# Optimization experiments

Measured on AMD Instinct MI355X. Metric: run time of the kernel, lower is better.

The kernel has to match this reference:

```python
import jax, jax.numpy as jnp
import numpy as np

V, D, NL, K, B, L, FF = 32000, 512, 4, 32, 2, 1024, 2048


def _ln(x, g, b, eps=1e-5):
    m = jnp.mean(x, axis=-1, keepdims=True)
    v = jnp.mean((x - m) ** 2, axis=-1, keepdims=True)
    return (x - m) * jax.lax.rsqrt(v + eps) * g + b


def setup_inputs() -> dict:
    key = jax.random.key(0)
    ks = jax.random.split(key, 16)
    s = 0.02
    n = lambda k, shape: jax.random.normal(k, shape, jnp.float32) * s
    inp = {
        "tokens": jax.random.randint(ks[0], (B, L), 0, V),
        "embed": n(ks[1], (V, D)),
        "ln1_g": jnp.ones((NL, D)), "ln1_b": jnp.zeros((NL, D)),
        "cp_w1": n(ks[2], (NL, D, D)), "cp_b1": jnp.zeros((NL, D)),
        "cp_w2": n(ks[3], (NL, D, K)), "cp_b2": jnp.zeros((NL, K)),
        "pos_scale": 0.5 * jnp.ones((NL,)), "content_scale": 0.5 * jnp.ones((NL,)),
        "val_w": n(ks[4], (NL, D, D)), "val_b": jnp.zeros((NL, D)),
        "oln_g": jnp.ones((NL, D)), "oln_b": jnp.zeros((NL, D)),
        "out_w": n(ks[5], (NL, D, D)), "out_b": jnp.zeros((NL, D)),
        "ln2_g": jnp.ones((NL, D)), "ln2_b": jnp.zeros((NL, D)),
        "ffn_w1": n(ks[6], (NL, D, FF)), "ffn_b1": jnp.zeros((NL, FF)),
        "ffn_w2": n(ks[7], (NL, FF, D)), "ffn_b2": jnp.zeros((NL, D)),
        "no_g": jnp.ones((D,)), "no_b": jnp.zeros((D,)),
        "head_b": jnp.zeros((V,)),
    }
    return inp


def _forward(tokens, embed, ln1_g, ln1_b, cp_w1, cp_b1, cp_w2, cp_b2,
             pos_scale, content_scale, val_w, val_b, oln_g, oln_b, out_w, out_b,
             ln2_g, ln2_b, ffn_w1, ffn_b1, ffn_w2, ffn_b2, no_g, no_b, head_b):
    Bn, Ln = tokens.shape
    Kn = cp_b2.shape[1]
    # fixed positional phases (register_buffer in torch)
    freqs = 1.0 / 10000.0 ** (jnp.arange(Kn, dtype=jnp.float32) / Kn)
    pos_phase = jnp.arange(Ln, dtype=jnp.float32)[:, None] * freqs[None, :]  # [L,K]
    inv_norm = 1.0 / jnp.sqrt(jnp.arange(1, Ln + 1, dtype=jnp.float32) * Kn)[None, :, None]
    h = embed[tokens]  # [B,L,D]
    for i in range(ln1_g.shape[0]):
        # --- DualAddressingPhasor on normed input ---
        x = _ln(h, ln1_g[i], ln1_b[i])
        cp = jnp.tanh(jnp.tanh(x @ cp_w1[i] + cp_b1[i]) @ cp_w2[i] + cp_b2[i]) * jnp.pi  # [B,L,K]
        tp = pos_scale[i] * pos_phase[None] + content_scale[i] * cp
        v = x @ val_w[i] + val_b[i]  # [B,L,D]
        c, s_ = jnp.cos(tp), jnp.sin(tp)  # [B,L,K]
        mem_r = jnp.cumsum(c[..., None] * v[:, :, None, :], axis=1)  # [B,L,K,D]
        mem_i = jnp.cumsum(s_[..., None] * v[:, :, None, :], axis=1)
        retrieved = (jnp.einsum('blkd,blk->bld', mem_r, c)
                     + jnp.einsum('blkd,blk->bld', mem_i, s_)) * inv_norm
        # phasor returns x + to_out(retrieved); block adds it back to h
        h = h + x + (_ln(retrieved, oln_g[i], oln_b[i]) @ out_w[i] + out_b[i])
        # --- FFN ---
        y = _ln(h, ln2_g[i], ln2_b[i])
        h = h + jax.nn.gelu(y @ ffn_w1[i] + ffn_b1[i], approximate=False) @ ffn_w2[i] + ffn_b2[i]
    # tied output head: head.weight = embed.weight
    return _ln(h, no_g, no_b) @ embed.T + head_b


def reference(tokens, embed, ln1_g, ln1_b, cp_w1, cp_b1, cp_w2, cp_b2,
              pos_scale, content_scale, val_w, val_b, oln_g, oln_b, out_w, out_b,
              ln2_g, ln2_b, ffn_w1, ffn_b1, ffn_w2, ffn_b2, no_g, no_b, head_b):
    return _forward(tokens, embed, ln1_g, ln1_b, cp_w1, cp_b1, cp_w2, cp_b2,
                    pos_scale, content_scale, val_w, val_b, oln_g, oln_b, out_w, out_b,
                    ln2_g, ln2_b, ffn_w1, ffn_b1, ffn_w2, ffn_b2, no_g, no_b, head_b)
```

## Files before the change

kernel.cpp:

```cpp
#include <hip/hip_runtime.h>
#include <hip/hip_bf16.h>
#include <math.h>

#define V_  32000
#define D_  512
#define NL_ 4
#define K_  32
#define B_  2
#define L_  1024
#define FF_ 2048
#define MR_ (B_ * L_)

typedef __bf16 bf16_t;
typedef __bf16 bf16x8 __attribute__((ext_vector_type(8)));
typedef float  f32x4  __attribute__((ext_vector_type(4)));

#define FLAG_TANH   1
#define FLAG_GELU   2
#define FLAG_INV    8
#define FLAG_CAUSAL 16
#define FLAG_TANHLO 32

#define GLDS(gsrc, ldst) \
  __builtin_amdgcn_global_load_lds( \
      (const __attribute__((address_space(1))) unsigned int*)(const void*)(gsrc), \
      (__attribute__((address_space(3))) unsigned int*)(void*)(ldst), 16, 0, 0)

__global__ void gather_kernel(const int* __restrict__ tokens,
                              const float* __restrict__ embed,
                              float* __restrict__ h) {
    int row = blockIdx.x;
    int t = tokens[row];
    const float4* src = (const float4*)(embed + (size_t)t * D_);
    float4* dst = (float4*)(h + (size_t)row * D_);
    dst[threadIdx.x] = src[threadIdx.x];
}

__global__ __launch_bounds__(256) void cvt_kernel(const float* __restrict__ in,
                                                  bf16_t* __restrict__ out) {
    size_t i = ((size_t)blockIdx.x * 256 + threadIdx.x) * 8;
    float4 f0 = ((const float4*)(in + i))[0];
    float4 f1 = ((const float4*)(in + i))[1];
    bf16x8 ov;
    ov[0] = (bf16_t)f0.x; ov[1] = (bf16_t)f0.y;
    ov[2] = (bf16_t)f0.z; ov[3] = (bf16_t)f0.w;
    ov[4] = (bf16_t)f1.x; ov[5] = (bf16_t)f1.y;
    ov[6] = (bf16_t)f1.z; ov[7] = (bf16_t)f1.w;
    *(bf16x8*)(out + i) = ov;
}

__global__ void bconcat_kernel(const float* __restrict__ a,
                               const float* __restrict__ b,
                               float* __restrict__ o) {
    int i = blockIdx.x, t = threadIdx.x;
    o[(size_t)i * 2 * D_ + t]       = a[(size_t)i * D_ + t];
    o[(size_t)i * 2 * D_ + D_ + t]  = b[(size_t)i * D_ + t];
}

__global__ __launch_bounds__(256) void ln_kernel(const float* __restrict__ in,
                                                 const float* __restrict__ g,
                                                 const float* __restrict__ b,
                                                 float* __restrict__ outf,
                                                 bf16_t* __restrict__ outb) {
    int row = blockIdx.x, tid = threadIdx.x;
    const float* rp = in + (size_t)row * D_;
    float v0 = rp[tid], v1 = rp[tid + 256];
    float s = v0 + v1, q = v0 * v0 + v1 * v1;
#pragma unroll
    for (int o = 32; o > 0; o >>= 1) {
        s += __shfl_down(s, o, 64);
        q += __shfl_down(q, o, 64);
    }
    __shared__ float ss[4], sq[4];
    if ((tid & 63) == 0) { ss[tid >> 6] = s; sq[tid >> 6] = q; }
    __syncthreads();
    float ts = ss[0] + ss[1] + ss[2] + ss[3];
    float tq = sq[0] + sq[1] + sq[2] + sq[3];
    float mean = ts * (1.0f / D_);
    float var = tq * (1.0f / D_) - mean * mean;
    float rstd = rsqrtf(var + 1e-5f);
    float o0 = (v0 - mean) * rstd * g[tid] + b[tid];
    float o1 = (v1 - mean) * rstd * g[tid + 256] + b[tid + 256];
    if (outf) {
        outf[(size_t)row * D_ + tid]       = o0;
        outf[(size_t)row * D_ + tid + 256] = o1;
    }
    if (outb) {
        outb[(size_t)row * D_ + tid]       = (bf16_t)o0;
        outb[(size_t)row * D_ + tid + 256] = (bf16_t)o1;
    }
}

__global__ __launch_bounds__(256) void tconv_kernel(const float* __restrict__ in,
                                                    bf16_t* __restrict__ out,
                                                    int R, int C,
                                                    size_t inz, size_t outz) {
    __shared__ float t[32][33];
    const float* ip = in + (size_t)blockIdx.z * inz;
    bf16_t* op = out + (size_t)blockIdx.z * outz;
    int r0 = blockIdx.y * 32, c0 = blockIdx.x * 32;
    int tx = threadIdx.x & 31, ty = threadIdx.x >> 5;
#pragma unroll
    for (int rr = 0; rr < 4; ++rr)
        t[ty + rr * 8][tx] = ip[(size_t)(r0 + ty + rr * 8) * C + c0 + tx];
    __syncthreads();
#pragma unroll
    for (int rr = 0; rr < 4; ++rr)
        op[(size_t)(c0 + ty + rr * 8) * R + r0 + tx] = (bf16_t)t[tx][ty + rr * 8];
}

template<int BM, int BN, int NBUF, bool BF32>
__global__ __launch_bounds__(256) void mgemm(
    const bf16_t* __restrict__ A, const void* __restrict__ Bp,
    const float* __restrict__ bias, const float* __restrict__ res1,
    const float* __restrict__ res2, float* __restrict__ Cf,
    bf16_t* __restrict__ Cb, int M, int N, int Kd, int flags,
    long long strA, long long strB, long long strC, int swz) {
    __shared__ bf16_t sA[NBUF][BM * 32];
    __shared__ bf16_t sB[NBUF][BN * 32];
    const int tid = threadIdx.x;
    const int wave = tid >> 6, lane = tid & 63;
    const int lrow = lane & 15, quad = lane >> 4;
    int bx = blockIdx.x, by = blockIdx.y;
    if (swz) {
        int gx = gridDim.x, gy = gridDim.y;
        int nwg = gx * gy;
        int lid = by * gx + bx;
        int q = nwg >> 3, r = nwg & 7;
        int xcd = lid & 7, slot = lid >> 3;
        int base = (xcd < r) ? xcd * (q + 1) : r * (q + 1) + (xcd - r) * q;
        int nid = base + slot;
        bx = nid / gy;
        by = nid - bx * gy;
    }
    const int m0 = by * BM, n0 = bx * BN;
    const int z = blockIdx.z;
    A += (size_t)z * strA;
    const bf16_t* Bb = (const bf16_t*)Bp + (BF32 ? 0 : (size_t)z * strB);
    const float*  Bf = (const float*)Bp  + (BF32 ? (size_t)z * strB : 0);
    constexpr int TM = BM / 32, TN = BN / 32;
    const int wm = (wave >> 1) * (BM / 2), wn = (wave & 1) * (BN / 2);
    f32x4 acc[TM][TN] = {};

    if constexpr (BF32) {
        for (int k0 = 0; k0 < Kd; k0 += 32) {
#pragma unroll
            for (int rb = 0; rb < BM / 64; ++rb) {
                int rowblk = wave * (BM / 64) + rb;
                int ml = rowblk * 16 + (lane >> 2);
                int qs = (lane & 3) ^ ((ml >> 1) & 3);
                GLDS(A + (size_t)(m0 + ml) * Kd + k0 + qs * 8, &sA[0][rowblk * 512]);
            }
#pragma unroll
            for (int rb = 0; rb < (BN * 4) / 256; ++rb) {
                int s = rb * 256 + tid;
                int nl = s >> 2, ql = s & 3;
                int qs = ql ^ ((nl >> 1) & 3);
                const float* src = Bf + (size_t)(n0 + nl) * Kd + k0 + qs * 8;
                float4 f0 = ((const float4*)src)[0];
                float4 f1 = ((const float4*)src)[1];
                bf16x8 ov;
                ov[0] = (bf16_t)f0.x; ov[1] = (bf16_t)f0.y;
                ov[2] = (bf16_t)f0.z; ov[3] = (bf16_t)f0.w;
                ov[4] = (bf16_t)f1.x; ov[5] = (bf16_t)f1.y;
                ov[6] = (bf16_t)f1.z; ov[7] = (bf16_t)f1.w;
                *(bf16x8*)(&sB[0][s * 8]) = ov;
            }
            __syncthreads();
            bf16x8 af[TM], bv[TN];
#pragma unroll
            for (int i = 0; i < TM; ++i) {
                int row = wm + i * 16 + lrow;
                af[i] = *(const bf16x8*)(&sA[0][(row * 4 + (quad ^ ((row >> 1) & 3))) * 8]);
            }
#pragma unroll
            for (int j = 0; j < TN; ++j) {
                int rown = wn + j * 16 + lrow;
                bv[j] = *(const bf16x8*)(&sB[0][(rown * 4 + (quad ^ ((rown >> 1) & 3))) * 8]);
            }
#pragma unroll
            for (int i = 0; i < TM; ++i)
#pragma unroll
                for (int j = 0; j < TN; ++j)
                    acc[i][j] = __builtin_amdgcn_mfma_f32_16x16x32_bf16(af[i], bv[j], acc[i][j], 0, 0, 0);
            __syncthreads();
        }
    } else {
        int kend = Kd;
        if (flags & FLAG_CAUSAL) { int ke = m0 + BM; kend = ke < Kd ? ke : Kd; }
        const int nk = kend >> 5;
        constexpr int NLD = BM / 64 + BN / 64;
        auto stage = [&](int t) {
            const int buf = t & (NBUF - 1);
            const int k0 = t << 5;
#pragma unroll
            for (int rb = 0; rb < BM / 64; ++rb) {
                int rowblk = wave * (BM / 64) + rb;
                int ml = rowblk * 16 + (lane >> 2);
                int qs = (lane & 3) ^ ((ml >> 1) & 3);
                GLDS(A + (size_t)(m0 + ml) * Kd + k0 + qs * 8, &sA[buf][rowblk * 512]);
            }
#pragma unroll
            for (int rb = 0; rb < BN / 64; ++rb) {
                int rowblk = wave * (BN / 64) + rb;
                int nl = rowblk * 16 + (lane >> 2);
                int qs = (lane & 3) ^ ((nl >> 1) & 3);
                GLDS(Bb + (size_t)(n0 + nl) * Kd + k0 + qs * 8, &sB[buf][rowblk * 512]);
            }
        };
        for (int t = 0; t < NBUF - 1 && t < nk; ++t) stage(t);
        for (int t = 0; t < nk; ++t) {
            const int nxt = t + NBUF - 1;
            if (nxt < nk) stage(nxt);
            const int issued_last = (nxt < nk) ? nxt : nk - 1;
            const int ahead = issued_last - t;
            switch (ahead) {
              case 0: asm volatile("s_waitcnt vmcnt(0)" ::: "memory"); break;
              case 1: asm volatile("s_waitcnt vmcnt(%0)" :: "n"(1 * NLD) : "memory"); break;
              case 2: asm volatile("s_waitcnt vmcnt(%0)" :: "n"(2 * NLD) : "memory"); break;
              default: asm volatile("s_waitcnt vmcnt(%0)" :: "n"(3 * NLD) : "memory"); break;
            }
            __builtin_amdgcn_s_barrier();
            const int buf = t & (NBUF - 1);
            const bf16_t* sAc = sA[buf];
            const bf16_t* sBc = sB[buf];
            bf16x8 af[TM], bv[TN];
#pragma unroll
            for (int i = 0; i < TM; ++i) {
                int row = wm + i * 16 + lrow;
                af[i] = *(const bf16x8*)(sAc + (row * 4 + (quad ^ ((row >> 1) & 3))) * 8);
            }
#pragma unroll
            for (int j = 0; j < TN; ++j) {
                int rown = wn + j * 16 + lrow;
                bv[j] = *(const bf16x8*)(sBc + (rown * 4 + (quad ^ ((rown >> 1) & 3))) * 8);
            }
#pragma unroll
            for (int i = 0; i < TM; ++i)
#pragma unroll
                for (int j = 0; j < TN; ++j)
                    acc[i][j] = __builtin_amdgcn_mfma_f32_16x16x32_bf16(af[i], bv[j], acc[i][j], 0, 0, 0);
            asm volatile("s_waitcnt lgkmcnt(0)" ::: "memory");
            __builtin_amdgcn_s_barrier();
        }
    }

    const size_t zo = (size_t)z * strC;
#pragma unroll
    for (int i = 0; i < TM; ++i) {
#pragma unroll
        for (int reg = 0; reg < 4; ++reg) {
            int m = m0 + wm + i * 16 + quad * 4 + reg;
            float rs = (flags & FLAG_INV) ? rsqrtf((float)(m + 1) * (float)K_) : 1.0f;
#pragma unroll
            for (int j = 0; j < TN; ++j) {
                int n = n0 + wn + j * 16 + lrow;
                float vv = acc[i][j][reg];
                if (bias) vv += bias[n];
                vv *= rs;
                if (flags & FLAG_TANH) vv = tanhf(vv);
                else if (flags & FLAG_GELU) vv = 0.5f * vv * (1.0f + erff(vv * 0.7071067811865476f));
                else if (flags & FLAG_TANHLO) { if (n < D_) vv = tanhf(vv); }
                size_t idx = zo + (size_t)m * N + n;
                if (res1) vv += res1[idx];
                if (res2) vv += res2[idx];
                if (Cf) Cf[idx] = vv;
                if (Cb) Cb[idx] = (bf16_t)vv;
            }
        }
    }
}

__global__ void phase_kernel(const float* __restrict__ t1,
                             const float* __restrict__ w2,
                             const float* __restrict__ b2,
                             const float* __restrict__ ps,
                             const float* __restrict__ cs,
                             int layer,
                             float* __restrict__ cbuf,
                             float* __restrict__ sbuf) {
    int row = blockIdx.x;
    int l = row & (L_ - 1);
    int tid = threadIdx.x;
    int k = tid & 31, hh = tid >> 5;
    const float* tr = t1 + (size_t)row * (2 * D_);
    float acc = 0.f;
    for (int d = hh * 256; d < hh * 256 + 256; ++d)
        acc = fmaf(tr[d], w2[d * K_ + k], acc);
    __shared__ float red[64];
    red[tid] = acc;
    __syncthreads();
    if (hh == 0) {
        float zz = red[k] + red[k + 32] + b2[k];
        float cp = tanhf(zz) * 3.14159265358979323846f;
        float freq = expf(-(float)k * (9.210340371976184f / (float)K_));
        float tp = ps[layer] * (float)l * freq + cs[layer] * cp;
        cbuf[(size_t)row * K_ + k] = cosf(tp);
        sbuf[(size_t)row * K_ + k] = sinf(tp);
    }
}

__global__ __launch_bounds__(256) void score_kernel(const float* __restrict__ cbuf,
                                                    const float* __restrict__ sbuf,
                                                    bf16_t* __restrict__ Ab) {
    int b = blockIdx.z;
    int l0 = blockIdx.y * 16, j0 = blockIdx.x * 16;
    if (j0 > l0) return;
    int tx = threadIdx.x, ty = threadIdx.y;
    int tid = ty * 16 + tx;
    __shared__ float Cl[16][33], Sl[16][33], Cj[16][33], Sj[16][33];
    const float* cb = cbuf + (size_t)b * L_ * K_;
    const float* sb = sbuf + (size_t)b * L_ * K_;
    for (int q = tid; q < 16 * 32; q += 256) {
        int rr = q >> 5, kk = q & 31;
        Cl[rr][kk] = cb[(size_t)(l0 + rr) * K_ + kk];
        Sl[rr][kk] = sb[(size_t)(l0 + rr) * K_ + kk];
        Cj[rr][kk] = cb[(size_t)(j0 + rr) * K_ + kk];
        Sj[rr][kk] = sb[(size_t)(j0 + rr) * K_ + kk];
    }
    __syncthreads();
    int l = l0 + ty, j = j0 + tx;
    float acc = 0.f;
#pragma unroll
    for (int kk = 0; kk < 32; ++kk)
        acc += Cl[ty][kk] * Cj[tx][kk] + Sl[ty][kk] * Sj[tx][kk];
    Ab[((size_t)b * L_ + l) * L_ + j] = (bf16_t)((j <= l) ? acc : 0.f);
}

extern "C" void kernel_launch(void* const* d_in, const int* in_sizes, int n_in,
                              void* d_out, int out_size, void* d_ws, size_t ws_size,
                              hipStream_t stream) {
    const int*   tokens        = (const int*)d_in[0];
    const float* embed         = (const float*)d_in[1];
    const float* ln1_g         = (const float*)d_in[2];
    const float* ln1_b         = (const float*)d_in[3];
    const float* cp_w1         = (const float*)d_in[4];
    const float* cp_b1         = (const float*)d_in[5];
    const float* cp_w2         = (const float*)d_in[6];
    const float* cp_b2         = (const float*)d_in[7];
    const float* pos_scale     = (const float*)d_in[8];
    const float* content_scale = (const float*)d_in[9];
    const float* val_w         = (const float*)d_in[10];
    const float* val_b         = (const float*)d_in[11];
    const float* oln_g         = (const float*)d_in[12];
    const float* oln_b         = (const float*)d_in[13];
    const float* out_w         = (const float*)d_in[14];
    const float* out_b         = (const float*)d_in[15];
    const float* ln2_g         = (const float*)d_in[16];
    const float* ln2_b         = (const float*)d_in[17];
    const float* ffn_w1        = (const float*)d_in[18];
    const float* ffn_b1        = (const float*)d_in[19];
    const float* ffn_w2        = (const float*)d_in[20];
    const float* ffn_b2        = (const float*)d_in[21];
    const float* no_g          = (const float*)d_in[22];
    const float* no_b          = (const float*)d_in[23];
    const float* head_b        = (const float*)d_in[24];
    float* out = (float*)d_out;

    float* h   = out;
    float* x   = h  + (size_t)MR_ * D_;
    float* t1v = x  + (size_t)MR_ * D_;
    float* r   = t1v + (size_t)MR_ * 2 * D_;
    float* cb  = r  + (size_t)MR_ * D_;
    float* sb  = cb + (size_t)MR_ * K_;
    bf16_t* x_bf  = (bf16_t*)(sb + (size_t)MR_ * K_);
    bf16_t* r_bf  = x_bf  + (size_t)MR_ * D_;
    bf16_t* y_bf  = r_bf  + (size_t)MR_ * D_;
    bf16_t* ff_bf = y_bf  + (size_t)MR_ * D_;
    bf16_t* sc_bf = ff_bf + (size_t)MR_ * FF_;
    bf16_t* vT_bf = sc_bf + (size_t)B_ * L_ * L_;
    bf16_t* wvT   = vT_bf + (size_t)B_ * D_ * L_;
    bf16_t* owT   = wvT   + (size_t)NL_ * 2 * D_ * D_;
    bf16_t* f1T   = owT   + (size_t)NL_ * D_ * D_;
    bf16_t* f2T   = f1T   + (size_t)NL_ * FF_ * D_;
    float*  b1v   = (float*)((((uintptr_t)(f2T + (size_t)NL_ * D_ * FF_)) + 15) & ~(uintptr_t)15);
    bf16_t* hn_bf = (bf16_t*)d_ws;
    bf16_t* emb_bf = hn_bf + (size_t)MR_ * D_;
    const bool big_ws =
        ws_size >= ((size_t)MR_ * D_ + (size_t)V_ * D_) * sizeof(bf16_t);

    gather_kernel<<<MR_, 128, 0, stream>>>(tokens, embed, h);

    tconv_kernel<<<dim3(16, 16, NL_), 256, 0, stream>>>(cp_w1, wvT, D_, D_, (size_t)D_ * D_, (size_t)2 * D_ * D_);
    tconv_kernel<<<dim3(16, 16, NL_), 256, 0, stream>>>(val_w, wvT + (size_t)D_ * D_, D_, D_, (size_t)D_ * D_, (size_t)2 * D_ * D_);
    bconcat_kernel<<<NL_, 512, 0, stream>>>(cp_b1, val_b, b1v);
    tconv_kernel<<<dim3(16, 16, NL_), 256, 0, stream>>>(out_w, owT, D_, D_, (size_t)D_ * D_, (size_t)D_ * D_);
    tconv_kernel<<<dim3(64, 16, NL_), 256, 0, stream>>>(ffn_w1, f1T, D_, FF_, (size_t)D_ * FF_, (size_t)D_ * FF_);
    tconv_kernel<<<dim3(16, 64, NL_), 256, 0, stream>>>(ffn_w2, f2T, FF_, D_, (size_t)FF_ * D_, (size_t)FF_ * D_);
    if (big_ws)
        cvt_kernel<<<(V_ * D_) / 2048, 256, 0, stream>>>(embed, emb_bf);

    for (int i = 0; i < NL_; ++i) {
        ln_kernel<<<MR_, 256, 0, stream>>>(h, ln1_g + i * D_, ln1_b + i * D_, x, x_bf);
        mgemm<64, 64, 4, false><<<dim3(16, 32, 1), 256, 0, stream>>>(
            x_bf, wvT + (size_t)i * 2 * D_ * D_, b1v + (size_t)i * 2 * D_,
            nullptr, nullptr, t1v, nullptr, MR_, 2 * D_, D_, FLAG_TANHLO, 0, 0, 0, 1);
        phase_kernel<<<MR_, 64, 0, stream>>>(
            t1v, cp_w2 + (size_t)i * D_ * K_, cp_b2 + i * K_,
            pos_scale, content_scale, i, cb, sb);
        tconv_kernel<<<dim3(16, 32, B_), 256, 0, stream>>>(
            t1v + D_, vT_bf, L_, 2 * D_, (size_t)L_ * 2 * D_, (size_t)D_ * L_);
        score_kernel<<<dim3(L_ / 16, L_ / 16, B_), dim3(16, 16), 0, stream>>>(cb, sb, sc_bf);
        mgemm<64, 64, 4, false><<<dim3(8, 16, B_), 256, 0, stream>>>(
            sc_bf, vT_bf, nullptr, nullptr, nullptr, r, nullptr,
            L_, D_, L_, FLAG_INV | FLAG_CAUSAL,
            (long long)L_ * L_, (long long)D_ * L_, (long long)L_ * D_, 1);
        ln_kernel<<<MR_, 256, 0, stream>>>(r, oln_g + i * D_, oln_b + i * D_, nullptr, r_bf);
        mgemm<64, 64, 4, false><<<dim3(8, 32, 1), 256, 0, stream>>>(
            r_bf, owT + (size_t)i * D_ * D_, out_b + i * D_,
            h, x, h, nullptr, MR_, D_, D_, 0, 0, 0, 0, 1);
        ln_kernel<<<MR_, 256, 0, stream>>>(h, ln2_g + i * D_, ln2_b + i * D_, nullptr, y_bf);
        mgemm<128, 128, 4, false><<<dim3(16, 16, 1), 256, 0, stream>>>(
            y_bf, f1T + (size_t)i * FF_ * D_, ffn_b1 + i * FF_,
            nullptr, nullptr, nullptr, ff_bf, MR_, FF_, D_, FLAG_GELU, 0, 0, 0, 1);
        mgemm<64, 64, 4, false><<<dim3(8, 32, 1), 256, 0, stream>>>(
            ff_bf, f2T + (size_t)i * D_ * FF_, ffn_b2 + i * D_,
            h, nullptr, h, nullptr, MR_, D_, FF_, 0, 0, 0, 0, 1);
    }

    ln_kernel<<<MR_, 256, 0, stream>>>(h, no_g, no_b, nullptr, hn_bf);
    if (big_ws) {
        mgemm<128, 128, 2, false><<<dim3(V_ / 128, MR_ / 128, 1), 256, 0, stream>>>(
            hn_bf, emb_bf, head_b, nullptr, nullptr, out, nullptr,
            MR_, V_, D_, 0, 0, 0, 0, 1);
    } else {
        mgemm<128, 128, 1, true><<<dim3(V_ / 128, MR_ / 128, 1), 256, 0, stream>>>(
            hn_bf, embed, head_b, nullptr, nullptr, out, nullptr,
            MR_, V_, D_, 0, 0, 0, 0, 1);
    }
}
```

Before: 1.508 ms.

## Compute phasor score matrix with MFMA GEMM over packed bf16 cos/sin

The phase kernel now writes cos and sin as one packed bf16 [row,64] buffer. The scalar fp32 score kernel is replaced by an mgemm call (csb times csb transposed, K=64) that skips upper-triangular tiles and zeroes entries where n>m. mgemm gains a dedicated two-buffer pipeline path so this short-K GEMM can use NBUF=2. This moves the score computation onto matrix cores, at the cost of rounding the cos/sin inputs to bf16 before the dot product, which lowers precision.

```diff
diff --git a/kernel.cpp b/kernel.cpp
--- a/kernel.cpp
+++ b/kernel.cpp
@@ -20,6 +20,7 @@
 #define FLAG_INV    8
 #define FLAG_CAUSAL 16
 #define FLAG_TANHLO 32
+#define FLAG_TRI    64
 
 #define GLDS(gsrc, ldst) \
   __builtin_amdgcn_global_load_lds( \
@@ -133,6 +134,7 @@
         bx = nid / gy;
         by = nid - bx * gy;
     }
+    if ((flags & FLAG_TRI) && bx > by) return;
     const int m0 = by * BM, n0 = bx * BN;
     const int z = blockIdx.z;
     A += (size_t)z * strA;
@@ -190,8 +192,7 @@
         if (flags & FLAG_CAUSAL) { int ke = m0 + BM; kend = ke < Kd ? ke : Kd; }
         const int nk = kend >> 5;
         constexpr int NLD = BM / 64 + BN / 64;
-        auto stage = [&](int t) {
-            const int buf = t & (NBUF - 1);
+        auto stage = [&](int t, int buf) {
             const int k0 = t << 5;
 #pragma unroll
             for (int rb = 0; rb < BM / 64; ++rb) {
@@ -208,20 +209,7 @@
                 GLDS(Bb + (size_t)(n0 + nl) * Kd + k0 + qs * 8, &sB[buf][rowblk * 512]);
             }
         };
-        for (int t = 0; t < NBUF - 1 && t < nk; ++t) stage(t);
-        for (int t = 0; t < nk; ++t) {
-            const int nxt = t + NBUF - 1;
-            if (nxt < nk) stage(nxt);
-            const int issued_last = (nxt < nk) ? nxt : nk - 1;
-            const int ahead = issued_last - t;
-            switch (ahead) {
-              case 0: asm volatile("s_waitcnt vmcnt(0)" ::: "memory"); break;
-              case 1: asm volatile("s_waitcnt vmcnt(%0)" :: "n"(1 * NLD) : "memory"); break;
-              case 2: asm volatile("s_waitcnt vmcnt(%0)" :: "n"(2 * NLD) : "memory"); break;
-              default: asm volatile("s_waitcnt vmcnt(%0)" :: "n"(3 * NLD) : "memory"); break;
-            }
-            __builtin_amdgcn_s_barrier();
-            const int buf = t & (NBUF - 1);
+        auto compute = [&](int buf) {
             const bf16_t* sAc = sA[buf];
             const bf16_t* sBc = sB[buf];
             bf16x8 af[TM], bv[TN];
@@ -240,8 +228,41 @@
 #pragma unroll
                 for (int j = 0; j < TN; ++j)
                     acc[i][j] = __builtin_amdgcn_mfma_f32_16x16x32_bf16(af[i], bv[j], acc[i][j], 0, 0, 0);
-            asm volatile("s_waitcnt lgkmcnt(0)" ::: "memory");
-            __builtin_amdgcn_s_barrier();
+        };
+        if constexpr (NBUF == 2) {
+            stage(0, 0);
+            int cur = 0;
+            for (int t = 0; t < nk; ++t) {
+                if (t + 1 < nk) {
+                    stage(t + 1, cur ^ 1);
+                    asm volatile("s_waitcnt vmcnt(%0)" :: "n"(NLD) : "memory");
+                } else {
+                    asm volatile("s_waitcnt vmcnt(0)" ::: "memory");
+                }
+                __builtin_amdgcn_s_barrier();
+                compute(cur);
+                asm volatile("s_waitcnt lgkmcnt(0)" ::: "memory");
+                __builtin_amdgcn_s_barrier();
+                cur ^= 1;
+            }
+        } else {
+            for (int t = 0; t < NBUF - 1 && t < nk; ++t) stage(t, t & (NBUF - 1));
+            for (int t = 0; t < nk; ++t) {
+                const int nxt = t + NBUF - 1;
+                if (nxt < nk) stage(nxt, nxt & (NBUF - 1));
+                const int issued_last = (nxt < nk) ? nxt : nk - 1;
+                const int ahead = issued_last - t;
+                switch (ahead) {
+                  case 0: asm volatile("s_waitcnt vmcnt(0)" ::: "memory"); break;
+                  case 1: asm volatile("s_waitcnt vmcnt(%0)" :: "n"(1 * NLD) : "memory"); break;
+                  case 2: asm volatile("s_waitcnt vmcnt(%0)" :: "n"(2 * NLD) : "memory"); break;
+                  default: asm volatile("s_waitcnt vmcnt(%0)" :: "n"(3 * NLD) : "memory"); break;
+                }
+                __builtin_amdgcn_s_barrier();
+                compute(t & (NBUF - 1));
+                asm volatile("s_waitcnt lgkmcnt(0)" ::: "memory");
+                __builtin_amdgcn_s_barrier();
+            }
         }
     }
 
@@ -261,6 +282,7 @@
                 if (flags & FLAG_TANH) vv = tanhf(vv);
                 else if (flags & FLAG_GELU) vv = 0.5f * vv * (1.0f + erff(vv * 0.7071067811865476f));
                 else if (flags & FLAG_TANHLO) { if (n < D_) vv = tanhf(vv); }
+                if ((flags & FLAG_TRI) && n > m) vv = 0.f;
                 size_t idx = zo + (size_t)m * N + n;
                 if (res1) vv += res1[idx];
                 if (res2) vv += res2[idx];
@@ -277,8 +299,7 @@
                              const float* __restrict__ ps,
                              const float* __restrict__ cs,
                              int layer,
-                             float* __restrict__ cbuf,
-                             float* __restrict__ sbuf) {
+                             bf16_t* __restrict__ csb) {
     int row = blockIdx.x;
     int l = row & (L_ - 1);
     int tid = threadIdx.x;
@@ -295,36 +316,9 @@
         float cp = tanhf(zz) * 3.14159265358979323846f;
         float freq = expf(-(float)k * (9.210340371976184f / (float)K_));
         float tp = ps[layer] * (float)l * freq + cs[layer] * cp;
-        cbuf[(size_t)row * K_ + k] = cosf(tp);
-        sbuf[(size_t)row * K_ + k] = sinf(tp);
-    }
-}
-
-__global__ __launch_bounds__(256) void score_kernel(const float* __restrict__ cbuf,
-                                                    const float* __restrict__ sbuf,
-                                                    bf16_t* __restrict__ Ab) {
-    int b = blockIdx.z;
-    int l0 = blockIdx.y * 16, j0 = blockIdx.x * 16;
-    if (j0 > l0) return;
-    int tx = threadIdx.x, ty = threadIdx.y;
-    int tid = ty * 16 + tx;
-    __shared__ float Cl[16][33], Sl[16][33], Cj[16][33], Sj[16][33];
-    const float* cb = cbuf + (size_t)b * L_ * K_;
-    const float* sb = sbuf + (size_t)b * L_ * K_;
-    for (int q = tid; q < 16 * 32; q += 256) {
-        int rr = q >> 5, kk = q & 31;
-        Cl[rr][kk] = cb[(size_t)(l0 + rr) * K_ + kk];
-        Sl[rr][kk] = sb[(size_t)(l0 + rr) * K_ + kk];
-        Cj[rr][kk] = cb[(size_t)(j0 + rr) * K_ + kk];
-        Sj[rr][kk] = sb[(size_t)(j0 + rr) * K_ + kk];
-    }
-    __syncthreads();
-    int l = l0 + ty, j = j0 + tx;
-    float acc = 0.f;
-#pragma unroll
-    for (int kk = 0; kk < 32; ++kk)
-        acc += Cl[ty][kk] * Cj[tx][kk] + Sl[ty][kk] * Sj[tx][kk];
-    Ab[((size_t)b * L_ + l) * L_ + j] = (bf16_t)((j <= l) ? acc : 0.f);
+        csb[(size_t)row * 64 + k]      = (bf16_t)cosf(tp);
+        csb[(size_t)row * 64 + 32 + k] = (bf16_t)sinf(tp);
+    }
 }
 
 extern "C" void kernel_launch(void* const* d_in, const int* in_sizes, int n_in,
@@ -361,19 +355,18 @@
     float* x   = h  + (size_t)MR_ * D_;
     float* t1v = x  + (size_t)MR_ * D_;
     float* r   = t1v + (size_t)MR_ * 2 * D_;
-    float* cb  = r  + (size_t)MR_ * D_;
-    float* sb  = cb + (size_t)MR_ * K_;
-    bf16_t* x_bf  = (bf16_t*)(sb + (size_t)MR_ * K_);
+    bf16_t* x_bf  = (bf16_t*)(r + (size_t)MR_ * D_);
     bf16_t* r_bf  = x_bf  + (size_t)MR_ * D_;
     bf16_t* y_bf  = r_bf  + (size_t)MR_ * D_;
     bf16_t* ff_bf = y_bf  + (size_t)MR_ * D_;
     bf16_t* sc_bf = ff_bf + (size_t)MR_ * FF_;
     bf16_t* vT_bf = sc_bf + (size_t)B_ * L_ * L_;
-    bf16_t* wvT   = vT_bf + (size_t)B_ * D_ * L_;
+    bf16_t* csb   = vT_bf + (size_t)B_ * D_ * L_;
+    bf16_t* wvT   = csb   + (size_t)MR_ * 64;
     bf16_t* owT   = wvT   + (size_t)NL_ * 2 * D_ * D_;
     bf16_t* f1T   = owT   + (size_t)NL_ * D_ * D_;
     bf16_t* f2T   = f1T   + (size_t)NL_ * FF_ * D_;
-    float*  b1v   = (float*)((((uintptr_t)(f2T + (size_t)NL_ * D_ * FF_)) + 15) & ~(uintptr_t)15);
+    float*  b1v   = (float*)(f2T + (size_t)NL_ * D_ * FF_);
     bf16_t* hn_bf = (bf16_t*)d_ws;
     bf16_t* emb_bf = hn_bf + (size_t)MR_ * D_;
     const bool big_ws =
@@ -397,10 +390,13 @@
             nullptr, nullptr, t1v, nullptr, MR_, 2 * D_, D_, FLAG_TANHLO, 0, 0, 0, 1);
         phase_kernel<<<MR_, 64, 0, stream>>>(
             t1v, cp_w2 + (size_t)i * D_ * K_, cp_b2 + i * K_,
-            pos_scale, content_scale, i, cb, sb);
+            pos_scale, content_scale, i, csb);
         tconv_kernel<<<dim3(16, 32, B_), 256, 0, stream>>>(
             t1v + D_, vT_bf, L_, 2 * D_, (size_t)L_ * 2 * D_, (size_t)D_ * L_);
-        score_kernel<<<dim3(L_ / 16, L_ / 16, B_), dim3(16, 16), 0, stream>>>(cb, sb, sc_bf);
+        mgemm<64, 64, 2, false><<<dim3(L_ / 64, L_ / 64, B_), 256, 0, stream>>>(
+            csb, csb, nullptr, nullptr, nullptr, nullptr, sc_bf,
+            L_, L_, 64, FLAG_TRI,
+            (long long)L_ * 64, (long long)L_ * 64, (long long)L_ * L_, 0);
         mgemm<64, 64, 4, false><<<dim3(8, 16, B_), 256, 0, stream>>>(
             sc_bf, vT_bf, nullptr, nullptr, nullptr, r, nullptr,
             L_, D_, L_, FLAG_INV | FLAG_CAUSAL,
```

New measurement: 1.489 ms. About the same (-1.3%).
